# Kernel optimization log

Measured on AMD Instinct MI355X. Metric: run time of the kernel, lower is better.

Reference implementation:

```python
import jax, jax.numpy as jnp
import numpy as np

N_NODES = 10000
N_EDGES = 160000
NEG_SLOPE = 0.2


def setup_inputs() -> dict:
    key = jax.random.key(0)
    ks = jax.random.split(key, 24)

    def rn(k, shape, scale):
        return (jax.random.normal(k, shape, dtype=jnp.float32) * scale)

    inp = {
        "x": rn(ks[0], (N_NODES, 128), 1.0),
        "edge_index": jax.random.randint(ks[1], (2, N_EDGES), 0, N_NODES, dtype=jnp.int32),
        "edge_attr": rn(ks[2], (N_EDGES, 8), 1.0),
        # GATConv 1: 128 -> 64 (heads=1)
        "W1": rn(ks[3], (128, 64), 0.09), "as1": rn(ks[4], (64,), 0.1), "ad1": rn(ks[5], (64,), 0.1), "b1": rn(ks[6], (64,), 0.01),
        # GATConv 2: 64 -> 256
        "W2": rn(ks[7], (64, 256), 0.125), "as2": rn(ks[8], (256,), 0.06), "ad2": rn(ks[9], (256,), 0.06), "b2": rn(ks[10], (256,), 0.01),
        # GATConv 3: 256 -> 1024
        "W3": rn(ks[11], (256, 1024), 0.0625), "as3": rn(ks[12], (1024,), 0.03), "ad3": rn(ks[13], (1024,), 0.03), "b3": rn(ks[14], (1024,), 0.01),
        # Dense head
        "lw1": rn(ks[15], (1024, 512), 0.03), "lb1": rn(ks[16], (512,), 0.01),
        "lw2": rn(ks[17], (512, 10), 0.04), "lb2": rn(ks[18], (10,), 0.01),
    }
    return inp


def gat_layer(x, src, dst, W, a_s, a_d, b, n):
    """PyG GATConv, heads=1, concat=True, add_self_loops handled by caller via src/dst."""
    h = x @ W                                   # [N, F_out]
    e = jax.nn.leaky_relu((h @ a_s)[src] + (h @ a_d)[dst], NEG_SLOPE)  # [E']
    m = jax.ops.segment_max(e, dst, num_segments=n)
    ex = jnp.exp(e - m[dst])
    denom = jax.ops.segment_sum(ex, dst, num_segments=n)
    alpha = ex / denom[dst]                     # scatter-softmax over incoming edges
    out = jax.ops.segment_sum(alpha[:, None] * h[src], dst, num_segments=n)
    return out + b


def reference(x, edge_index, edge_attr, W1, as1, ad1, b1, W2, as2, ad2, b2,
              W3, as3, ad3, b3, lw1, lb1, lw2, lb2):
    # edge_attr is accepted but ignored (GATConv built without edge_dim)
    n = x.shape[0]
    loops = jnp.arange(n, dtype=edge_index.dtype)  # add_self_loops=True
    src = jnp.concatenate([edge_index[0], loops])
    dst = jnp.concatenate([edge_index[1], loops])

    h = jax.nn.relu(gat_layer(x, src, dst, W1, as1, ad1, b1, n))
    h = jax.nn.relu(gat_layer(h, src, dst, W2, as2, ad2, b2, n))
    h = jax.nn.relu(gat_layer(h, src, dst, W3, as3, ad3, b3, n))

    pooled = jnp.max(h, axis=0, keepdims=True)  # global_max_pool, batch=None -> [1, 1024]
    z = jax.nn.relu(pooled @ lw1 + lb1)
    z = z @ lw2 + lb2
    return jax.nn.log_softmax(z, axis=1)
```

## Files before the change

### kernel.cpp

```cpp
#include <hip/hip_runtime.h>
#include <hip/hip_bf16.h>
#include <math.h>

#define NEG_SLOPE 0.2f
typedef unsigned short u16;
typedef short bf16x8 __attribute__((ext_vector_type(8)));
typedef float f32x4 __attribute__((ext_vector_type(4)));

__device__ __forceinline__ float bfu2f(u16 u) { return __uint_as_float(((unsigned)u) << 16); }
__device__ __forceinline__ u16 f2bu(float v) { return __bfloat16_as_ushort(__float2bfloat16(v)); }

__global__ void prep_kernel(int* deg, int* cursor, float* pooled, int N,
                            const float* __restrict__ x, u16* __restrict__ xb,
                            const float* __restrict__ W1, u16* __restrict__ Wt1,
                            const float* __restrict__ W2, u16* __restrict__ Wt2,
                            const float* __restrict__ W3, u16* __restrict__ Wt3,
                            const float* __restrict__ as2, const float* __restrict__ ad2,
                            const float* __restrict__ as3, const float* __restrict__ ad3,
                            float* __restrict__ ws2, float* __restrict__ wd2,
                            float* __restrict__ ws3, float* __restrict__ wd3,
                            int c0, int c1, int c2, int c3, int c4) {
    int bid = blockIdx.x, tid = threadIdx.x;
    if (bid < c0) {
        int i = bid * 256 + tid;
        if (i < N) { deg[i] = 0; cursor[i] = 0; }
        if (i < 1024) pooled[i] = 0.f;
    } else if (bid < c1) {
        int i = (bid - c0) * 256 + tid;
        if (i < N * 128) xb[i] = f2bu(x[i]);
    } else if (bid < c2) {
        int i = (bid - c1) * 256 + tid;
        int k = i % 128, f = i / 128;
        Wt1[i] = f2bu(W1[k * 64 + f]);
    } else if (bid < c3) {
        int i = (bid - c2) * 256 + tid;
        int k = i % 64, f = i / 64;
        Wt2[i] = f2bu(W2[k * 256 + f]);
    } else if (bid < c4) {
        int i = (bid - c3) * 256 + tid;
        int k = i % 256, f = i / 256;
        Wt3[i] = f2bu(W3[(size_t)k * 1024 + f]);
    } else {
        int wv = ((bid - c4) * 256 + tid) >> 6;
        int lane = tid & 63;
        const float *W, *va, *vd; float *os, *od; int F, row;
        if (wv < 64) { W = W2; va = as2; vd = ad2; F = 256; row = wv; os = ws2; od = wd2; }
        else if (wv < 320) { W = W3; va = as3; vd = ad3; F = 1024; row = wv - 64; os = ws3; od = wd3; }
        else return;
        const float* wr = W + (size_t)row * F;
        float ss = 0.f, dd = 0.f;
        for (int f = lane; f < F; f += 64) { float wvv = wr[f]; ss += wvv * va[f]; dd += wvv * vd[f]; }
        for (int off = 32; off; off >>= 1) { ss += __shfl_xor(ss, off); dd += __shfl_xor(dd, off); }
        if (lane == 0) { os[row] = ss; od[row] = dd; }
    }
}

__global__ void count_kernel(const int* __restrict__ edst, int E, int N, int* deg) {
    int i = blockIdx.x * blockDim.x + threadIdx.x;
    int total = E + N;
    if (i >= total) return;
    int dn = (i < E) ? edst[i] : (i - E);
    atomicAdd(&deg[dn], 1);
}

__global__ void scan_kernel(const int* __restrict__ deg, int N, int* __restrict__ offsets) {
    __shared__ int part[257];
    int tid = threadIdx.x;
    int chunk = (N + 255) / 256;
    int begin = tid * chunk;
    int fin = begin + chunk; if (fin > N) fin = N; if (begin > N) begin = N;
    int sum = 0;
    for (int i = begin; i < fin; ++i) sum += deg[i];
    part[tid] = sum;
    __syncthreads();
    if (tid == 0) {
        int acc = 0;
        for (int t = 0; t < 256; ++t) { int v = part[t]; part[t] = acc; acc += v; }
        part[256] = acc;
    }
    __syncthreads();
    int acc = part[tid];
    for (int i = begin; i < fin; ++i) { offsets[i] = acc; acc += deg[i]; }
    if (tid == 255) offsets[N] = part[256];
}

__global__ void scatter_kernel(const int* __restrict__ esrc, const int* __restrict__ edst,
                               int E, int N, const int* __restrict__ offsets,
                               int* cursor, int* __restrict__ srcg) {
    int i = blockIdx.x * blockDim.x + threadIdx.x;
    int total = E + N;
    if (i >= total) return;
    int sn, dn;
    if (i < E) { sn = esrc[i]; dn = edst[i]; } else { sn = i - E; dn = i - E; }
    int pos = atomicAdd(&cursor[dn], 1);
    srcg[offsets[dn] + pos] = sn;
}

template <int K, int MR, bool BIASRELU, bool SD_EPI>
__global__ __launch_bounds__(256) void mfma_gemm(const u16* __restrict__ A,
                                                 const u16* __restrict__ Wt,
                                                 u16* __restrict__ C,
                                                 const float* __restrict__ bias,
                                                 int M, int F,
                                                 const float* __restrict__ asv,
                                                 const float* __restrict__ adv,
                                                 float* __restrict__ s_out,
                                                 float* __restrict__ d_out) {
    constexpr int NK = K / 32;
    int tid = threadIdx.x;
    int w = tid >> 6, l = tid & 63;
    int l15 = l & 15, q = l >> 4;
    int bm = blockIdx.x * (64 * MR);
    int bn = blockIdx.y * 64;
    int r0 = bm + w * (16 * MR);

    const u16* aptr[MR];
    int row[MR];
#pragma unroll
    for (int mr = 0; mr < MR; ++mr) {
        int r = r0 + mr * 16 + l15;
        row[mr] = r;
        int ar = (r < M) ? r : (M - 1);
        aptr[mr] = A + (size_t)ar * K + 8 * q;
    }
    const u16* bptr[4];
#pragma unroll
    for (int nt = 0; nt < 4; ++nt)
        bptr[nt] = Wt + (size_t)(bn + nt * 16 + l15) * K + 8 * q;

    f32x4 acc[MR][4];
#pragma unroll
    for (int mr = 0; mr < MR; ++mr)
#pragma unroll
        for (int nt = 0; nt < 4; ++nt) acc[mr][nt] = (f32x4){0.f, 0.f, 0.f, 0.f};

    bf16x8 a_cur[MR], b_cur[4], a_nxt[MR], b_nxt[4];
#pragma unroll
    for (int mr = 0; mr < MR; ++mr) a_cur[mr] = *(const bf16x8*)(aptr[mr]);
#pragma unroll
    for (int nt = 0; nt < 4; ++nt) b_cur[nt] = *(const bf16x8*)(bptr[nt]);

#pragma unroll
    for (int kk = 0; kk < NK; ++kk) {
        if (kk + 1 < NK) {
            int koff = (kk + 1) * 32;
#pragma unroll
            for (int mr = 0; mr < MR; ++mr) a_nxt[mr] = *(const bf16x8*)(aptr[mr] + koff);
#pragma unroll
            for (int nt = 0; nt < 4; ++nt) b_nxt[nt] = *(const bf16x8*)(bptr[nt] + koff);
        }
#pragma unroll
        for (int mr = 0; mr < MR; ++mr)
#pragma unroll
            for (int nt = 0; nt < 4; ++nt)
                acc[mr][nt] = __builtin_amdgcn_mfma_f32_16x16x32_bf16(b_cur[nt], a_cur[mr], acc[mr][nt], 0, 0, 0);
        if (kk + 1 < NK) {
#pragma unroll
            for (int mr = 0; mr < MR; ++mr) a_cur[mr] = a_nxt[mr];
#pragma unroll
            for (int nt = 0; nt < 4; ++nt) b_cur[nt] = b_nxt[nt];
        }
    }

#pragma unroll
    for (int mr = 0; mr < MR; ++mr) {
        if (row[mr] >= M) continue;
#pragma unroll
        for (int nt = 0; nt < 4; ++nt) {
            int col = bn + nt * 16 + 4 * q;
            ushort4 st;
#pragma unroll
            for (int r = 0; r < 4; ++r) {
                float v = acc[mr][nt][r];
                if (BIASRELU) { v += bias[col + r]; v = fmaxf(v, 0.f); }
                ((u16*)&st)[r] = f2bu(v);
            }
            *(ushort4*)(C + (size_t)row[mr] * F + col) = st;
        }
    }

    if constexpr (SD_EPI) {
        float ss = 0.f, dd = 0.f;
#pragma unroll
        for (int nt = 0; nt < 4; ++nt)
#pragma unroll
            for (int r = 0; r < 4; ++r) {
                int col = nt * 16 + 4 * q + r;
                float v = acc[0][nt][r];
                ss += v * asv[col];
                dd += v * adv[col];
            }
        ss += __shfl_xor(ss, 16); ss += __shfl_xor(ss, 32);
        dd += __shfl_xor(dd, 16); dd += __shfl_xor(dd, 32);
        if (q == 0 && row[0] < M) { s_out[row[0]] = ss; d_out[row[0]] = dd; }
    }
}

__global__ __launch_bounds__(512) void gemm3_kernel(const u16* __restrict__ A,
                                                    const u16* __restrict__ Wt,
                                                    const float* __restrict__ bias,
                                                    int M,
                                                    float* __restrict__ pmaxbuf) {
    constexpr int K = 256;
    constexpr int NK = K / 32;
    __shared__ float pm[4][128];
    int tid = threadIdx.x;
    int w = tid >> 6, l = tid & 63;
    int w2 = w >> 1, wc = w & 1;
    int l15 = l & 15, q = l >> 4;
    int rb = blockIdx.x, cb = blockIdx.y;
    int bm = rb * 256;
    int bn = cb * 128 + wc * 64;

    const u16* aptr[4];
    int row[4];
#pragma unroll
    for (int mr = 0; mr < 4; ++mr) {
        int r = bm + w2 * 64 + mr * 16 + l15;
        row[mr] = r;
        int ar = (r < M) ? r : (M - 1);
        aptr[mr] = A + (size_t)ar * K + 8 * q;
    }
    const u16* bptr[4];
#pragma unroll
    for (int nt = 0; nt < 4; ++nt)
        bptr[nt] = Wt + (size_t)(bn + nt * 16 + l15) * K + 8 * q;

    f32x4 acc[4][4];
#pragma unroll
    for (int mr = 0; mr < 4; ++mr)
#pragma unroll
        for (int nt = 0; nt < 4; ++nt) acc[mr][nt] = (f32x4){0.f, 0.f, 0.f, 0.f};

    bf16x8 a_cur[4], b_cur[4], a_nxt[4], b_nxt[4];
#pragma unroll
    for (int mr = 0; mr < 4; ++mr) a_cur[mr] = *(const bf16x8*)(aptr[mr]);
#pragma unroll
    for (int nt = 0; nt < 4; ++nt) b_cur[nt] = *(const bf16x8*)(bptr[nt]);

#pragma unroll
    for (int kk = 0; kk < NK; ++kk) {
        if (kk + 1 < NK) {
            int koff = (kk + 1) * 32;
#pragma unroll
            for (int mr = 0; mr < 4; ++mr) a_nxt[mr] = *(const bf16x8*)(aptr[mr] + koff);
#pragma unroll
            for (int nt = 0; nt < 4; ++nt) b_nxt[nt] = *(const bf16x8*)(bptr[nt] + koff);
        }
#pragma unroll
        for (int mr = 0; mr < 4; ++mr)
#pragma unroll
            for (int nt = 0; nt < 4; ++nt)
                acc[mr][nt] = __builtin_amdgcn_mfma_f32_16x16x32_bf16(b_cur[nt], a_cur[mr], acc[mr][nt], 0, 0, 0);
        if (kk + 1 < NK) {
#pragma unroll
            for (int mr = 0; mr < 4; ++mr) a_cur[mr] = a_nxt[mr];
#pragma unroll
            for (int nt = 0; nt < 4; ++nt) b_cur[nt] = b_nxt[nt];
        }
    }

    float pmax[4][4];
#pragma unroll
    for (int nt = 0; nt < 4; ++nt)
#pragma unroll
        for (int r = 0; r < 4; ++r) pmax[nt][r] = 0.f;
#pragma unroll
    for (int mr = 0; mr < 4; ++mr) {
        bool valid = (row[mr] < M);
#pragma unroll
        for (int nt = 0; nt < 4; ++nt)
#pragma unroll
            for (int r = 0; r < 4; ++r) {
                float v = acc[mr][nt][r] + bias[bn + nt * 16 + 4 * q + r];
                v = fmaxf(v, 0.f);
                if (valid) pmax[nt][r] = fmaxf(pmax[nt][r], v);
            }
    }
#pragma unroll
    for (int nt = 0; nt < 4; ++nt)
#pragma unroll
        for (int r = 0; r < 4; ++r) {
#pragma unroll
            for (int msk = 1; msk < 16; msk <<= 1)
                pmax[nt][r] = fmaxf(pmax[nt][r], __shfl_xor(pmax[nt][r], msk));
        }
    if (l15 == 0) {
#pragma unroll
        for (int nt = 0; nt < 4; ++nt)
#pragma unroll
            for (int r = 0; r < 4; ++r)
                pm[w2][wc * 64 + nt * 16 + 4 * q + r] = pmax[nt][r];
    }
    __syncthreads();
    if (tid < 128) {
        float v = fmaxf(fmaxf(pm[0][tid], pm[1][tid]), fmaxf(pm[2][tid], pm[3][tid]));
        pmaxbuf[(size_t)rb * 1024 + cb * 128 + tid] = v;
    }
}

__global__ void pool_reduce_kernel(const float* __restrict__ pmaxbuf, int nrb,
                                   float* __restrict__ pooled) {
    int f = blockIdx.x * 256 + threadIdx.x;
    float m = 0.f;
    for (int rb = 0; rb < nrb; ++rb) m = fmaxf(m, pmaxbuf[(size_t)rb * 1024 + f]);
    pooled[f] = m;
}

__global__ void sd_kernel(const u16* __restrict__ h, const float* __restrict__ a_s,
                          const float* __restrict__ a_d, int N, int F,
                          float* __restrict__ s, float* __restrict__ d) {
    int wave = (blockIdx.x * blockDim.x + threadIdx.x) >> 6;
    int lane = threadIdx.x & 63;
    if (wave >= N) return;
    const u16* hrow = h + (size_t)wave * F;
    float ss = 0.f, dd = 0.f;
    for (int f = lane * 4; f < F; f += 256) {
        ushort4 u = *reinterpret_cast<const ushort4*>(hrow + f);
        float4 av = *reinterpret_cast<const float4*>(a_s + f);
        float4 dv = *reinterpret_cast<const float4*>(a_d + f);
        float h0 = bfu2f(u.x), h1 = bfu2f(u.y), h2 = bfu2f(u.z), h3 = bfu2f(u.w);
        ss += h0 * av.x + h1 * av.y + h2 * av.z + h3 * av.w;
        dd += h0 * dv.x + h1 * dv.y + h2 * dv.z + h3 * dv.w;
    }
    for (int off = 32; off; off >>= 1) { ss += __shfl_xor(ss, off); dd += __shfl_xor(dd, off); }
    if (lane == 0) { s[wave] = ss; d[wave] = dd; }
}

template <int F, int FS, bool BIASRELU, bool SD_EPI>
__global__ __launch_bounds__(256) void agg_kernel(const u16* __restrict__ h,
                                                  const float* __restrict__ sv,
                                                  const float* __restrict__ dvec,
                                                  const int* __restrict__ srcg,
                                                  const int* __restrict__ offsets,
                                                  const float* __restrict__ bias,
                                                  u16* __restrict__ out,
                                                  const float* __restrict__ wsv,
                                                  const float* __restrict__ wdv,
                                                  float* __restrict__ s_out,
                                                  float* __restrict__ d_out) {
    constexpr int FB = F / FS;
    constexpr int VPT = FB / 64;
    __shared__ float pL[256];
    __shared__ int sL[256];
    __shared__ float red[3][FB];
    int n = blockIdx.x;
    int f0 = blockIdx.y * FB;
    int tid = threadIdx.x;
    int w = tid >> 6, lane = tid & 63;
    int start = offsets[n], end = offsets[n + 1];
    int deg = end - start;
    float dval = dvec[n];
    float acc[VPT];
#pragma unroll
    for (int v = 0; v < VPT; ++v) acc[v] = 0.f;
    float inv;

    auto gpoint = [&](int sn) { return h + (size_t)sn * F + f0 + lane * VPT; };
    auto accum = [&](float pw, const u16* hp) {
        if constexpr (VPT == 4) {
            ushort4 u = *(const ushort4*)hp;
            acc[0] += pw * bfu2f(u.x); acc[1] += pw * bfu2f(u.y);
            acc[2] += pw * bfu2f(u.z); acc[3] += pw * bfu2f(u.w);
        } else if constexpr (VPT == 2) {
            ushort2 u = *(const ushort2*)hp;
            acc[0] += pw * bfu2f(u.x); acc[1] += pw * bfu2f(u.y);
        } else {
            acc[0] += pw * bfu2f(*hp);
        }
    };

    if (deg <= 256) {
        float e = -INFINITY;
        if (tid < deg) {
            int sn = srcg[start + tid];
            sL[tid] = sn;
            float v = sv[sn] + dval;
            e = (v >= 0.f) ? v : NEG_SLOPE * v;
        }
        pL[tid] = e;
        __syncthreads();
        float m = fmaxf(fmaxf(pL[lane], pL[lane + 64]), fmaxf(pL[lane + 128], pL[lane + 192]));
#pragma unroll
        for (int off2 = 32; off2; off2 >>= 1) m = fmaxf(m, __shfl_xor(m, off2));
        __syncthreads();
        float p = (tid < deg) ? expf(e - m) : 0.f;
        pL[tid] = p;
        __syncthreads();
        float t4 = (pL[lane] + pL[lane + 64]) + (pL[lane + 128] + pL[lane + 192]);
#pragma unroll
        for (int off2 = 32; off2; off2 >>= 1) t4 += __shfl_xor(t4, off2);
        inv = 1.f / t4;
        int jj = w;
        for (; jj + 4 < deg; jj += 8) {
            float p0 = pL[jj], p1 = pL[jj + 4];
            const u16* h0 = gpoint(sL[jj]);
            const u16* h1 = gpoint(sL[jj + 4]);
            accum(p0, h0);
            accum(p1, h1);
        }
        if (jj < deg) accum(pL[jj], gpoint(sL[jj]));
    } else {
        float lmax = -INFINITY;
        for (int j = start + lane; j < end; j += 64) {
            float v = sv[srcg[j]] + dval; v = (v >= 0.f) ? v : NEG_SLOPE * v;
            lmax = fmaxf(lmax, v);
        }
#pragma unroll
        for (int off2 = 32; off2; off2 >>= 1) lmax = fmaxf(lmax, __shfl_xor(lmax, off2));
        float ls = 0.f;
        for (int j = start + lane; j < end; j += 64) {
            float v = sv[srcg[j]] + dval; v = (v >= 0.f) ? v : NEG_SLOPE * v;
            ls += expf(v - lmax);
        }
#pragma unroll
        for (int off2 = 32; off2; off2 >>= 1) ls += __shfl_xor(ls, off2);
        inv = 1.f / ls;
        for (int j = start + w; j < end; j += 4) {
            int sn = srcg[j];
            float e2 = sv[sn] + dval; e2 = (e2 >= 0.f) ? e2 : NEG_SLOPE * e2;
            accum(expf(e2 - lmax), gpoint(sn));
        }
    }

    if (w > 0) {
#pragma unroll
        for (int v = 0; v < VPT; ++v) red[w - 1][lane * VPT + v] = acc[v];
    }
    __syncthreads();
    if (w != 0) return;
    float res0 = 0.f;
    if constexpr (VPT == 2) {
        ushort2 st;
#pragma unroll
        for (int v = 0; v < VPT; ++v) {
            float xv = (acc[v] + red[0][lane * 2 + v] + red[1][lane * 2 + v] + red[2][lane * 2 + v]) * inv;
            if (BIASRELU) { xv += bias[f0 + lane * 2 + v]; xv = fmaxf(xv, 0.f); }
            ((u16*)&st)[v] = f2bu(xv);
        }
        *(ushort2*)(out + (size_t)n * F + f0 + lane * 2) = st;
    } else if constexpr (VPT == 1) {
        float xv = (acc[0] + red[0][lane] + red[1][lane] + red[2][lane]) * inv;
        if (BIASRELU) { xv += bias[f0 + lane]; xv = fmaxf(xv, 0.f); }
        res0 = xv;
        out[(size_t)n * F + f0 + lane] = f2bu(xv);
    } else {
        ushort4 st;
#pragma unroll
        for (int v = 0; v < VPT; ++v) {
            float xv = (acc[v] + red[0][lane * 4 + v] + red[1][lane * 4 + v] + red[2][lane * 4 + v]) * inv;
            if (BIASRELU) { xv += bias[f0 + lane * 4 + v]; xv = fmaxf(xv, 0.f); }
            ((u16*)&st)[v] = f2bu(xv);
        }
        *(ushort4*)(out + (size_t)n * F + f0 + lane * 4) = st;
    }
    if constexpr (SD_EPI) {
        float ss = res0 * wsv[lane], dd = res0 * wdv[lane];
        for (int off2 = 32; off2; off2 >>= 1) { ss += __shfl_xor(ss, off2); dd += __shfl_xor(dd, off2); }
        if (lane == 0) { s_out[n] = ss; d_out[n] = dd; }
    }
}

__global__ void head1a_kernel(const float* __restrict__ pooled, const float* __restrict__ lw1,
                              float* __restrict__ part) {
    int j = blockIdx.x * 128 + threadIdx.x;
    int k0 = blockIdx.y * 64;
    float acc = 0.f;
#pragma unroll 8
    for (int k = k0; k < k0 + 64; ++k) acc += pooled[k] * lw1[(size_t)k * 512 + j];
    part[blockIdx.y * 512 + j] = acc;
}

__global__ void head1bc_kernel(const float* __restrict__ part, const float* __restrict__ lb1,
                               const float* __restrict__ lw2, const float* __restrict__ lb2,
                               float* __restrict__ out) {
    __shared__ float zs[512];
    __shared__ float z2s[10];
    int tid = threadIdx.x;
    if (tid < 512) {
        float acc = lb1[tid];
#pragma unroll
        for (int t = 0; t < 16; ++t) acc += part[t * 512 + tid];
        zs[tid] = fmaxf(acc, 0.f);
    }
    __syncthreads();
    int w = tid >> 6, lane = tid & 63;
    if (w < 10) {
        float acc = 0.f;
#pragma unroll
        for (int kc = 0; kc < 8; ++kc) {
            int k = kc * 64 + lane;
            acc += zs[k] * lw2[k * 10 + w];
        }
        for (int off = 32; off; off >>= 1) acc += __shfl_xor(acc, off);
        if (lane == 0) z2s[w] = acc + lb2[w];
    }
    __syncthreads();
    if (tid == 0) {
        float m = z2s[0];
        for (int j = 1; j < 10; ++j) m = fmaxf(m, z2s[j]);
        float ssum = 0.f;
        for (int j = 0; j < 10; ++j) ssum += expf(z2s[j] - m);
        float lse = m + logf(ssum);
        for (int j = 0; j < 10; ++j) out[j] = z2s[j] - lse;
    }
}

extern "C" void kernel_launch(void* const* d_in, const int* in_sizes, int n_in,
                              void* d_out, int out_size, void* d_ws, size_t ws_size,
                              hipStream_t stream) {
    const float* x   = (const float*)d_in[0];
    const int* ei    = (const int*)d_in[1];
    const float* W1  = (const float*)d_in[3];
    const float* as1 = (const float*)d_in[4];
    const float* ad1 = (const float*)d_in[5];
    const float* b1  = (const float*)d_in[6];
    const float* W2  = (const float*)d_in[7];
    const float* as2 = (const float*)d_in[8];
    const float* ad2 = (const float*)d_in[9];
    const float* b2  = (const float*)d_in[10];
    const float* W3  = (const float*)d_in[11];
    const float* as3 = (const float*)d_in[12];
    const float* ad3 = (const float*)d_in[13];
    const float* b3  = (const float*)d_in[14];
    const float* lw1 = (const float*)d_in[15];
    const float* lb1 = (const float*)d_in[16];
    const float* lw2 = (const float*)d_in[17];
    const float* lb2 = (const float*)d_in[18];
    float* out = (float*)d_out;

    const int N = in_sizes[0] / 128;
    const int E = in_sizes[1] / 2;
    const int total = E + N;
    const int* esrc = ei;
    const int* edst = ei + E;

    char* base = (char*)d_ws;
    size_t off = 0;
    auto alloc = [&](size_t bytes) { void* p = base + off; off = (off + bytes + 255) & ~(size_t)255; return p; };
    u16* xb    = (u16*)alloc((size_t)N * 128 * 2);
    u16* h1    = (u16*)alloc((size_t)N * 64 * 2);
    u16* a1    = (u16*)alloc((size_t)N * 64 * 2);
    u16* agg2b = (u16*)alloc((size_t)N * 64 * 2);
    u16* a2    = (u16*)alloc((size_t)N * 256 * 2);
    u16* agg3b = (u16*)alloc((size_t)N * 256 * 2);
    u16* Wt1   = (u16*)alloc(128 * 64 * 2);
    u16* Wt2   = (u16*)alloc(64 * 256 * 2);
    u16* Wt3   = (u16*)alloc(256 * 1024 * 2);
    float* ws2 = (float*)alloc(64 * 4);
    float* wd2 = (float*)alloc(64 * 4);
    float* ws3 = (float*)alloc(256 * 4);
    float* wd3 = (float*)alloc(256 * 4);
    float* sbuf = (float*)alloc((size_t)N * 4);
    float* dbuf = (float*)alloc((size_t)N * 4);
    float* pooled = (float*)alloc(1024 * 4);
    float* hpart  = (float*)alloc(16 * 512 * 4);
    int* deg     = (int*)alloc((size_t)N * 4);
    int* cursor  = (int*)alloc((size_t)N * 4);
    int* offsets = (int*)alloc((size_t)(N + 1) * 4);
    int* srcg    = (int*)alloc((size_t)total * 4);
    int nrb256 = (N + 255) / 256;
    float* pmaxbuf = (float*)alloc((size_t)nrb256 * 1024 * 4);

    const int TPB = 256;
    int gE = (total + TPB - 1) / TPB;
    int gW = (N + 3) / 4;
    int gR64 = (N + 63) / 64;
    int gR128 = (N + 127) / 128;

    int c0 = (N + 255) / 256;
    int c1 = c0 + (N * 128 + 255) / 256;
    int c2 = c1 + (128 * 64) / 256;
    int c3 = c2 + (64 * 256) / 256;
    int c4 = c3 + (256 * 1024) / 256;
    int gP = c4 + 80;
    prep_kernel<<<gP, TPB, 0, stream>>>(deg, cursor, pooled, N, x, xb,
                                        W1, Wt1, W2, Wt2, W3, Wt3,
                                        as2, ad2, as3, ad3, ws2, wd2, ws3, wd3,
                                        c0, c1, c2, c3, c4);

    count_kernel<<<gE, TPB, 0, stream>>>(edst, E, N, deg);
    scan_kernel<<<1, TPB, 0, stream>>>(deg, N, offsets);
    scatter_kernel<<<gE, TPB, 0, stream>>>(esrc, edst, E, N, offsets, cursor, srcg);

    mfma_gemm<128, 1, false, true><<<dim3(gR64, 1), TPB, 0, stream>>>(
        xb, Wt1, h1, nullptr, N, 64, as1, ad1, sbuf, dbuf);
    agg_kernel<64, 1, true, true><<<dim3(N, 1), TPB, 0, stream>>>(
        h1, sbuf, dbuf, srcg, offsets, b1, a1, ws2, wd2, sbuf, dbuf);

    agg_kernel<64, 1, false, false><<<dim3(N, 1), TPB, 0, stream>>>(
        a1, sbuf, dbuf, srcg, offsets, nullptr, agg2b, nullptr, nullptr, nullptr, nullptr);
    mfma_gemm<64, 2, true, false><<<dim3(gR128, 4), TPB, 0, stream>>>(
        agg2b, Wt2, a2, b2, N, 256, nullptr, nullptr, nullptr, nullptr);

    sd_kernel<<<gW, TPB, 0, stream>>>(a2, ws3, wd3, N, 256, sbuf, dbuf);
    agg_kernel<256, 2, false, false><<<dim3(N, 2), TPB, 0, stream>>>(
        a2, sbuf, dbuf, srcg, offsets, nullptr, agg3b, nullptr, nullptr, nullptr, nullptr);
    gemm3_kernel<<<dim3(nrb256, 8), 512, 0, stream>>>(agg3b, Wt3, b3, N, pmaxbuf);
    pool_reduce_kernel<<<4, TPB, 0, stream>>>(pmaxbuf, nrb256, pooled);

    head1a_kernel<<<dim3(4, 16), 128, 0, stream>>>(pooled, lw1, hpart);
    head1bc_kernel<<<1, 640, 0, stream>>>(hpart, lb1, lw2, lb2, out);
}
```

Measured before the change: 193.6 us.

## Stage gemm3 tiles in LDS via async global_load_lds with XOR swizzle

Rewrites the layer-3 GEMM+maxpool kernel to load whole 128x256 A and B tiles into shared memory with direct global-to-LDS loads and an XOR swizzle, then run MFMA from LDS. The old version read each fragment straight from global memory. The tile shrinks from 256x128 to 128x128 with 8 waves in a 2x4 arrangement, which doubles the number of blocks, and each wave writes its partial max directly to a larger pmaxbuf instead of going through a block-level reduction. This trades 128KB of LDS per block (low occupancy) and a larger pool-reduce input for better cooperative, coalesced loads.

```diff
diff --git a/kernel.cpp b/kernel.cpp
--- a/kernel.cpp
+++ b/kernel.cpp
@@ -9,6 +9,11 @@
 
 __device__ __forceinline__ float bfu2f(u16 u) { return __uint_as_float(((unsigned)u) << 16); }
 __device__ __forceinline__ u16 f2bu(float v) { return __bfloat16_as_ushort(__float2bfloat16(v)); }
+
+__device__ __forceinline__ void gload_lds16(const void* g, void* l) {
+    __builtin_amdgcn_global_load_lds((const __attribute__((address_space(1))) void*)g,
+                                     (__attribute__((address_space(3))) void*)l, 16, 0, 0);
+}
 
 __global__ void prep_kernel(int* deg, int* cursor, float* pooled, int N,
                             const float* __restrict__ x, u16* __restrict__ xb,
@@ -202,83 +207,81 @@
                                                     int M,
                                                     float* __restrict__ pmaxbuf) {
     constexpr int K = 256;
-    constexpr int NK = K / 32;
-    __shared__ float pm[4][128];
+    constexpr int ABYTES = 128 * 512;
+    __shared__ char lds[2 * ABYTES];
     int tid = threadIdx.x;
-    int w = tid >> 6, l = tid & 63;
-    int w2 = w >> 1, wc = w & 1;
-    int l15 = l & 15, q = l >> 4;
-    int rb = blockIdx.x, cb = blockIdx.y;
-    int bm = rb * 256;
-    int bn = cb * 128 + wc * 64;
-
-    const u16* aptr[4];
-    int row[4];
+    int w = tid >> 6, lane = tid & 63;
+    int w2 = w >> 2, wc = w & 3;
+    int l15 = lane & 15, q = lane >> 4;
+    int bid = blockIdx.x;
+    int rb = bid >> 3, cb = bid & 7;
+    int bm = rb * 128, bn = cb * 128;
+
+#pragma unroll
+    for (int it = 0; it < 8; ++it) {
+        int c = it * 512 + tid;
+        int row = c >> 5, kc = c & 31;
+        int arow = bm + row; if (arow >= M) arow = M - 1;
+        gload_lds16(A + (size_t)arow * K + ((kc ^ (row & 7)) * 8),
+                    lds + (size_t)(it * 512 + (tid & ~63)) * 16);
+    }
+#pragma unroll
+    for (int it = 0; it < 8; ++it) {
+        int c = it * 512 + tid;
+        int col = c >> 5, kc = c & 31;
+        gload_lds16(Wt + (size_t)(bn + col) * K + ((kc ^ (col & 7)) * 8),
+                    lds + ABYTES + (size_t)(it * 512 + (tid & ~63)) * 16);
+    }
+    __syncthreads();
+
+    f32x4 acc[4][2];
+#pragma unroll
+    for (int mr = 0; mr < 4; ++mr)
+#pragma unroll
+        for (int nt = 0; nt < 2; ++nt) acc[mr][nt] = (f32x4){0.f, 0.f, 0.f, 0.f};
+
+    const char* abase = lds;
+    const char* bbase = lds + ABYTES;
+#pragma unroll
+    for (int kk = 0; kk < 8; ++kk) {
+        int c = kk * 4 + q;
+        bf16x8 af[4], bfr[2];
+#pragma unroll
+        for (int mr = 0; mr < 4; ++mr) {
+            int row = w2 * 64 + mr * 16 + l15;
+            af[mr] = *(const bf16x8*)(abase + row * 512 + ((c ^ (row & 7)) * 16));
+        }
+#pragma unroll
+        for (int nt = 0; nt < 2; ++nt) {
+            int col = wc * 32 + nt * 16 + l15;
+            bfr[nt] = *(const bf16x8*)(bbase + col * 512 + ((c ^ (col & 7)) * 16));
+        }
+#pragma unroll
+        for (int mr = 0; mr < 4; ++mr)
+#pragma unroll
+            for (int nt = 0; nt < 2; ++nt)
+                acc[mr][nt] = __builtin_amdgcn_mfma_f32_16x16x32_bf16(bfr[nt], af[mr], acc[mr][nt], 0, 0, 0);
+    }
+
+    float pmax[2][4];
+#pragma unroll
+    for (int nt = 0; nt < 2; ++nt)
+#pragma unroll
+        for (int r = 0; r < 4; ++r) pmax[nt][r] = 0.f;
 #pragma unroll
     for (int mr = 0; mr < 4; ++mr) {
-        int r = bm + w2 * 64 + mr * 16 + l15;
-        row[mr] = r;
-        int ar = (r < M) ? r : (M - 1);
-        aptr[mr] = A + (size_t)ar * K + 8 * q;
-    }
-    const u16* bptr[4];
-#pragma unroll
-    for (int nt = 0; nt < 4; ++nt)
-        bptr[nt] = Wt + (size_t)(bn + nt * 16 + l15) * K + 8 * q;
-
-    f32x4 acc[4][4];
-#pragma unroll
-    for (int mr = 0; mr < 4; ++mr)
-#pragma unroll
-        for (int nt = 0; nt < 4; ++nt) acc[mr][nt] = (f32x4){0.f, 0.f, 0.f, 0.f};
-
-    bf16x8 a_cur[4], b_cur[4], a_nxt[4], b_nxt[4];
-#pragma unroll
-    for (int mr = 0; mr < 4; ++mr) a_cur[mr] = *(const bf16x8*)(aptr[mr]);
-#pragma unroll
-    for (int nt = 0; nt < 4; ++nt) b_cur[nt] = *(const bf16x8*)(bptr[nt]);
-
-#pragma unroll
-    for (int kk = 0; kk < NK; ++kk) {
-        if (kk + 1 < NK) {
-            int koff = (kk + 1) * 32;
-#pragma unroll
-            for (int mr = 0; mr < 4; ++mr) a_nxt[mr] = *(const bf16x8*)(aptr[mr] + koff);
-#pragma unroll
-            for (int nt = 0; nt < 4; ++nt) b_nxt[nt] = *(const bf16x8*)(bptr[nt] + koff);
-        }
-#pragma unroll
-        for (int mr = 0; mr < 4; ++mr)
-#pragma unroll
-            for (int nt = 0; nt < 4; ++nt)
-                acc[mr][nt] = __builtin_amdgcn_mfma_f32_16x16x32_bf16(b_cur[nt], a_cur[mr], acc[mr][nt], 0, 0, 0);
-        if (kk + 1 < NK) {
-#pragma unroll
-            for (int mr = 0; mr < 4; ++mr) a_cur[mr] = a_nxt[mr];
-#pragma unroll
-            for (int nt = 0; nt < 4; ++nt) b_cur[nt] = b_nxt[nt];
-        }
-    }
-
-    float pmax[4][4];
-#pragma unroll
-    for (int nt = 0; nt < 4; ++nt)
-#pragma unroll
-        for (int r = 0; r < 4; ++r) pmax[nt][r] = 0.f;
-#pragma unroll
-    for (int mr = 0; mr < 4; ++mr) {
-        bool valid = (row[mr] < M);
-#pragma unroll
-        for (int nt = 0; nt < 4; ++nt)
+        bool valid = (bm + w2 * 64 + mr * 16 + l15) < M;
+#pragma unroll
+        for (int nt = 0; nt < 2; ++nt)
 #pragma unroll
             for (int r = 0; r < 4; ++r) {
-                float v = acc[mr][nt][r] + bias[bn + nt * 16 + 4 * q + r];
+                float v = acc[mr][nt][r] + bias[bn + wc * 32 + nt * 16 + 4 * q + r];
                 v = fmaxf(v, 0.f);
                 if (valid) pmax[nt][r] = fmaxf(pmax[nt][r], v);
             }
     }
 #pragma unroll
-    for (int nt = 0; nt < 4; ++nt)
+    for (int nt = 0; nt < 2; ++nt)
 #pragma unroll
         for (int r = 0; r < 4; ++r) {
 #pragma unroll
@@ -287,23 +290,18 @@
         }
     if (l15 == 0) {
 #pragma unroll
-        for (int nt = 0; nt < 4; ++nt)
+        for (int nt = 0; nt < 2; ++nt)
 #pragma unroll
             for (int r = 0; r < 4; ++r)
-                pm[w2][wc * 64 + nt * 16 + 4 * q + r] = pmax[nt][r];
-    }
-    __syncthreads();
-    if (tid < 128) {
-        float v = fmaxf(fmaxf(pm[0][tid], pm[1][tid]), fmaxf(pm[2][tid], pm[3][tid]));
-        pmaxbuf[(size_t)rb * 1024 + cb * 128 + tid] = v;
-    }
-}
-
-__global__ void pool_reduce_kernel(const float* __restrict__ pmaxbuf, int nrb,
+                pmaxbuf[(size_t)(rb * 2 + w2) * 1024 + bn + wc * 32 + nt * 16 + 4 * q + r] = pmax[nt][r];
+    }
+}
+
+__global__ void pool_reduce_kernel(const float* __restrict__ pmaxbuf, int nslices,
                                    float* __restrict__ pooled) {
     int f = blockIdx.x * 256 + threadIdx.x;
     float m = 0.f;
-    for (int rb = 0; rb < nrb; ++rb) m = fmaxf(m, pmaxbuf[(size_t)rb * 1024 + f]);
+    for (int s = 0; s < nslices; ++s) m = fmaxf(m, pmaxbuf[(size_t)s * 1024 + f]);
     pooled[f] = m;
 }
 
@@ -559,8 +557,8 @@
     int* cursor  = (int*)alloc((size_t)N * 4);
     int* offsets = (int*)alloc((size_t)(N + 1) * 4);
     int* srcg    = (int*)alloc((size_t)total * 4);
-    int nrb256 = (N + 255) / 256;
-    float* pmaxbuf = (float*)alloc((size_t)nrb256 * 1024 * 4);
+    int nrb128g = (N + 127) / 128;
+    float* pmaxbuf = (float*)alloc((size_t)nrb128g * 2 * 1024 * 4);
 
     const int TPB = 256;
     int gE = (total + TPB - 1) / TPB;
@@ -596,8 +594,8 @@
     sd_kernel<<<gW, TPB, 0, stream>>>(a2, ws3, wd3, N, 256, sbuf, dbuf);
     agg_kernel<256, 2, false, false><<<dim3(N, 2), TPB, 0, stream>>>(
         a2, sbuf, dbuf, srcg, offsets, nullptr, agg3b, nullptr, nullptr, nullptr, nullptr);
-    gemm3_kernel<<<dim3(nrb256, 8), 512, 0, stream>>>(agg3b, Wt3, b3, N, pmaxbuf);
-    pool_reduce_kernel<<<4, TPB, 0, stream>>>(pmaxbuf, nrb256, pooled);
+    gemm3_kernel<<<nrb128g * 8, 512, 0, stream>>>(agg3b, Wt3, b3, N, pmaxbuf);
+    pool_reduce_kernel<<<4, TPB, 0, stream>>>(pmaxbuf, nrb128g * 2, pooled);
 
     head1a_kernel<<<dim3(4, 16), 128, 0, stream>>>(pooled, lw1, hpart);
     head1bc_kernel<<<1, 640, 0, stream>>>(hpart, lb1, lw2, lb2, out);
```

Measured after the change: 193.1 us. No clear change (-0.3%).
